# Kernel optimization log

Measured on AMD Instinct MI355X. Metric: run time of the kernel, lower is better.

Reference implementation:

```python
import jax, jax.numpy as jnp
import numpy as np

N_NODES = 100000


def _gcn_norm(edge_index, num_nodes):
    # PyG GCNConv default: add self-loops, symmetric normalization
    src, dst = edge_index[0], edge_index[1]
    loop = jnp.arange(num_nodes, dtype=src.dtype)
    src = jnp.concatenate([src, loop])
    dst = jnp.concatenate([dst, loop])
    deg = jax.ops.segment_sum(jnp.ones_like(dst, dtype=jnp.float32), dst,
                              num_segments=num_nodes)
    dinv = jnp.where(deg > 0, jax.lax.rsqrt(deg), 0.0)
    norm = dinv[src] * dinv[dst]  # [E + N]
    return src, dst, norm


def _gcn_conv(x, W, b, src, dst, norm, num_nodes):
    h = x @ W                                   # [N, out] linear first (PyG)
    msg = h[src] * norm[:, None]                # gather + scale  [E+N, out]
    out = jax.ops.segment_sum(msg, dst, num_segments=num_nodes)  # scatter-add
    return out + b


def setup_inputs() -> dict:
    key = jax.random.key(0)
    ks = jax.random.split(key, 5)
    x = jax.random.normal(ks[0], (N_NODES, 3), dtype=jnp.float32)
    edge_index = jax.random.randint(ks[1], (2, 1600000), 0, N_NODES, dtype=jnp.int64)
    # Glorot-ish weights, zero bias (PyG defaults)
    W1 = jax.random.normal(ks[2], (3, 64), dtype=jnp.float32) * (1.0 / np.sqrt(3))
    W2 = jax.random.normal(ks[3], (64, 64), dtype=jnp.float32) * (1.0 / np.sqrt(64))
    W3 = jax.random.normal(ks[4], (64, 3), dtype=jnp.float32) * (1.0 / np.sqrt(64))
    b1 = jnp.zeros((64,), jnp.float32)
    b2 = jnp.zeros((64,), jnp.float32)
    b3 = jnp.zeros((3,), jnp.float32)
    return {"x": x, "edge_index": edge_index, "W1": W1, "b1": b1,
            "W2": W2, "b2": b2, "W3": W3, "b3": b3}


def reference(x, edge_index, W1, b1, W2, b2, W3, b3):
    n = x.shape[0]
    src, dst, norm = _gcn_norm(edge_index, n)  # same graph for every layer
    h = jax.nn.relu(_gcn_conv(x, W1, b1, src, dst, norm, n))
    h = jax.nn.relu(_gcn_conv(h, W2, b2, src, dst, norm, n))
    return _gcn_conv(h, W3, b3, src, dst, norm, n)
```

## Files before the change

kernel.cpp:

```cpp
#include <hip/hip_runtime.h>

#define TPB 256
#define NB 391
#define CH 8192
#define BS 4736


__device__ __forceinline__ unsigned bpack(float a, float b) {
    unsigned ua = __float_as_uint(a), ub = __float_as_uint(b);
    ua = (ua + 0x7fffu + ((ua >> 16) & 1u)) >> 16;
    ub = (ub + 0x7fffu + ((ub >> 16) & 1u)) >> 16;
    return ua | (ub << 16);
}
__device__ __forceinline__ float blo(unsigned u) { return __uint_as_float(u << 16); }
__device__ __forceinline__ float bhi(unsigned u) { return __uint_as_float(u & 0xffff0000u); }


__global__ __launch_bounds__(512) void k_init(unsigned* __restrict__ gcur) {
    int t = threadIdx.x;
    if (t < NB) gcur[t] = (unsigned)(t * BS);
}


__global__ __launch_bounds__(TPB) void k_placeA(const int* __restrict__ src,
                                                const int* __restrict__ dst,
                                                unsigned* __restrict__ gcur,
                                                unsigned* __restrict__ bkt, int E) {
    __shared__ unsigned val[CH];
    __shared__ unsigned short bid[CH];
    __shared__ unsigned cnt[512], loff[512], lcur[512], basev[512];
    __shared__ unsigned tsum[TPB];
    int t = threadIdx.x;
    int c0 = blockIdx.x * CH;
    int n = E - c0; if (n > CH) n = CH;

    for (int b = t; b < 512; b += TPB) { cnt[b] = 0; lcur[b] = 0; }
    __syncthreads();
    for (int i = t; i < n; i += TPB)
        atomicAdd(&cnt[(unsigned)dst[c0 + i] >> 8], 1u);
    __syncthreads();
    for (int b = t; b < NB; b += TPB)
        basev[b] = cnt[b] ? atomicAdd(&gcur[b], cnt[b]) : 0u;
    unsigned a0 = cnt[2 * t], a1 = cnt[2 * t + 1];
    tsum[t] = a0 + a1;
    __syncthreads();
#pragma unroll
    for (int o = 1; o < TPB; o <<= 1) {
        unsigned v = (t >= o) ? tsum[t - o] : 0u;
        __syncthreads();
        tsum[t] += v;
        __syncthreads();
    }
    unsigned ex = tsum[t] - (a0 + a1);
    loff[2 * t] = ex; loff[2 * t + 1] = ex + a0;
    __syncthreads();
    for (int i = t; i < n; i += TPB) {
        unsigned s = (unsigned)src[c0 + i];
        unsigned d = (unsigned)dst[c0 + i];
        unsigned b = d >> 8;
        unsigned r = atomicAdd(&lcur[b], 1u);
        unsigned slot = loff[b] + r;
        val[slot] = s | ((d & 255u) << 20);
        bid[slot] = (unsigned short)b;
    }
    __syncthreads();
    for (int i = t; i < n; i += TPB) {
        unsigned b = bid[i];
        bkt[basev[b] + ((unsigned)i - loff[b])] = val[i];
    }
}


__global__ __launch_bounds__(TPB) void k_fineS(const unsigned* __restrict__ bkt,
                                               const unsigned* __restrict__ gcur,
                                               const float* __restrict__ x,
                                               int2* __restrict__ rp2,
                                               int* __restrict__ ssrc,
                                               float* __restrict__ dinv,
                                               float4* __restrict__ xs4, int N) {
    __shared__ unsigned cnt[256], sc[256], off[256];
    int t = threadIdx.x, b = blockIdx.x;
    cnt[t] = 0;
    __syncthreads();
    int p0 = b * BS, p1 = (int)gcur[b];
    for (int i = p0 + t; i < p1; i += TPB)
        atomicAdd(&cnt[bkt[i] >> 20], 1u);
    __syncthreads();
    unsigned c = cnt[t];
    sc[t] = c;
    __syncthreads();
#pragma unroll
    for (int o = 1; o < 256; o <<= 1) {
        unsigned v = (t >= o) ? sc[t - o] : 0u;
        __syncthreads();
        sc[t] += v;
        __syncthreads();
    }
    unsigned ex = sc[t] - c;
    off[t] = (unsigned)p0 + ex;
    int node = (b << 8) + t;
    if (node < N) {
        int beg = p0 + (int)ex;
        rp2[node] = make_int2(beg, beg + (int)c);
        float dv = rsqrtf((float)(c + 1u));
        dinv[node] = dv;
        float4 xv;
        xv.x = x[node * 3 + 0] * dv;
        xv.y = x[node * 3 + 1] * dv;
        xv.z = x[node * 3 + 2] * dv;
        xv.w = 0.f;
        xs4[node] = xv;
    }
    __syncthreads();
    for (int i = p0 + t; i < p1; i += TPB) {
        unsigned u = bkt[i];
        unsigned r = atomicAdd(&off[u >> 20], 1u);
        ssrc[r] = (int)(u & 0xFFFFFu);
    }
}


__global__ __launch_bounds__(TPB) void k_l1f2(const float4* __restrict__ xs4,
                                              const int2* __restrict__ rp2,
                                              const int* __restrict__ ssrc,
                                              const float* __restrict__ dinv,
                                              const float* __restrict__ W1,
                                              const float* __restrict__ b1,
                                              const float* __restrict__ W2,
                                              uint4* __restrict__ gb, int N) {
    int node = blockIdx.x * TPB + threadIdx.x;
    if (node >= N) return;
    int2 r = rp2[node];
    int beg = r.x, end = r.y;
    float4 q = xs4[node];
    int j = beg;
    for (; j + 3 < end; j += 4) {
        int s0 = ssrc[j], s1 = ssrc[j+1], s2 = ssrc[j+2], s3 = ssrc[j+3];
        float4 v0 = xs4[s0], v1 = xs4[s1], v2 = xs4[s2], v3 = xs4[s3];
        q.x += (v0.x + v1.x) + (v2.x + v3.x);
        q.y += (v0.y + v1.y) + (v2.y + v3.y);
        q.z += (v0.z + v1.z) + (v2.z + v3.z);
    }
    for (; j < end; ++j) {
        float4 v = xs4[ssrc[j]];
        q.x += v.x; q.y += v.y; q.z += v.z;
    }
    float dv = dinv[node];
    float q0 = q.x * dv, q1 = q.y * dv, q2 = q.z * dv;

    float acc[64];
#pragma unroll
    for (int f = 0; f < 64; ++f) acc[f] = 0.f;
    for (int kb = 0; kb < 16; ++kb) {
        int k0 = __builtin_amdgcn_readfirstlane(kb) << 2;
        const float* W1k = W1 + k0;
        const float* b1k = b1 + k0;
        float4 hv;
        hv.x = fmaxf(fmaf(q0, W1k[0], fmaf(q1, W1k[64], fmaf(q2, W1k[128], b1k[0]))), 0.f);
        hv.y = fmaxf(fmaf(q0, W1k[1], fmaf(q1, W1k[65], fmaf(q2, W1k[129], b1k[1]))), 0.f);
        hv.z = fmaxf(fmaf(q0, W1k[2], fmaf(q1, W1k[66], fmaf(q2, W1k[130], b1k[2]))), 0.f);
        hv.w = fmaxf(fmaf(q0, W1k[3], fmaf(q1, W1k[67], fmaf(q2, W1k[131], b1k[3]))), 0.f);
        const float* Wr = W2 + (k0 << 6);
#pragma unroll
        for (int f = 0; f < 64; ++f) {
            float a = acc[f];
            a = fmaf(hv.x, Wr[f],        a);
            a = fmaf(hv.y, Wr[64  + f],  a);
            a = fmaf(hv.z, Wr[128 + f],  a);
            a = fmaf(hv.w, Wr[192 + f],  a);
            acc[f] = a;
        }
    }
#pragma unroll
    for (int g8 = 0; g8 < 8; ++g8) {
        uint4 v;
        v.x = bpack(acc[8*g8+0] * dv, acc[8*g8+1] * dv);
        v.y = bpack(acc[8*g8+2] * dv, acc[8*g8+3] * dv);
        v.z = bpack(acc[8*g8+4] * dv, acc[8*g8+5] * dv);
        v.w = bpack(acc[8*g8+6] * dv, acc[8*g8+7] * dv);
        gb[((size_t)node << 3) + g8] = v;
    }
}


__global__ __launch_bounds__(TPB) void k_p2fb(const uint4* __restrict__ gb,
                                              const int2* __restrict__ rp2,
                                              const int* __restrict__ ssrc,
                                              const float* __restrict__ dinv,
                                              const float* __restrict__ b2,
                                              const float* __restrict__ W3,
                                              float* __restrict__ q4, int N) {
    int tid = blockIdx.x * TPB + threadIdx.x;
    int node = tid >> 3, q = tid & 7;
    if (node >= N) return;
    int2 r = rp2[node];
    int beg = r.x, end = r.y;
    float a[8];
    {
        uint4 u = gb[((size_t)node << 3) + q];
        a[0] = blo(u.x); a[1] = bhi(u.x);
        a[2] = blo(u.y); a[3] = bhi(u.y);
        a[4] = blo(u.z); a[5] = bhi(u.z);
        a[6] = blo(u.w); a[7] = bhi(u.w);
    }
    int j = beg;
    for (; j + 3 < end; j += 4) {
        int s0 = ssrc[j], s1 = ssrc[j+1], s2 = ssrc[j+2], s3 = ssrc[j+3];
        uint4 u0 = gb[((size_t)s0 << 3) + q];
        uint4 u1 = gb[((size_t)s1 << 3) + q];
        uint4 u2 = gb[((size_t)s2 << 3) + q];
        uint4 u3 = gb[((size_t)s3 << 3) + q];
        a[0] += (blo(u0.x) + blo(u1.x)) + (blo(u2.x) + blo(u3.x));
        a[1] += (bhi(u0.x) + bhi(u1.x)) + (bhi(u2.x) + bhi(u3.x));
        a[2] += (blo(u0.y) + blo(u1.y)) + (blo(u2.y) + blo(u3.y));
        a[3] += (bhi(u0.y) + bhi(u1.y)) + (bhi(u2.y) + bhi(u3.y));
        a[4] += (blo(u0.z) + blo(u1.z)) + (blo(u2.z) + blo(u3.z));
        a[5] += (bhi(u0.z) + bhi(u1.z)) + (bhi(u2.z) + bhi(u3.z));
        a[6] += (blo(u0.w) + blo(u1.w)) + (blo(u2.w) + blo(u3.w));
        a[7] += (bhi(u0.w) + bhi(u1.w)) + (bhi(u2.w) + bhi(u3.w));
    }
    for (; j < end; ++j) {
        uint4 u = gb[((size_t)ssrc[j] << 3) + q];
        a[0] += blo(u.x); a[1] += bhi(u.x);
        a[2] += blo(u.y); a[3] += bhi(u.y);
        a[4] += blo(u.z); a[5] += bhi(u.z);
        a[6] += blo(u.w); a[7] += bhi(u.w);
    }
    float dv = dinv[node];
    int f0 = q << 3;
    const float* bb = b2 + f0;
    const float* Wr = W3 + f0 * 3;
    float p0 = 0.f, p1 = 0.f, p2 = 0.f;
#pragma unroll
    for (int i = 0; i < 8; ++i) {
        float h = fmaxf(fmaf(a[i], dv, bb[i]), 0.f);
        p0 = fmaf(h, Wr[3*i+0], p0);
        p1 = fmaf(h, Wr[3*i+1], p1);
        p2 = fmaf(h, Wr[3*i+2], p2);
    }
#pragma unroll
    for (int off = 1; off < 8; off <<= 1) {
        p0 += __shfl_xor(p0, off, 64);
        p1 += __shfl_xor(p1, off, 64);
        p2 += __shfl_xor(p2, off, 64);
    }
    if (q < 4) {
        float v = (q == 0) ? p0 * dv : (q == 1) ? p1 * dv : (q == 2) ? p2 * dv : 0.f;
        q4[((size_t)node << 2) + q] = v;
    }
}


__global__ __launch_bounds__(TPB) void k_pull3o(const float* __restrict__ g34,
                                                const int2* __restrict__ rp2,
                                                const int* __restrict__ ssrc,
                                                const float* __restrict__ dinv,
                                                const float* __restrict__ b3,
                                                float* __restrict__ out, int N) {
    int tid = blockIdx.x * TPB + threadIdx.x;
    int node = tid >> 2, c = tid & 3;
    if (node >= N) return;
    int2 r = rp2[node];
    int beg = r.x, end = r.y;
    float acc = g34[tid];
    int j = beg;
    for (; j + 3 < end; j += 4) {
        int s0 = ssrc[j], s1 = ssrc[j+1], s2 = ssrc[j+2], s3 = ssrc[j+3];
        acc += (g34[(s0 << 2) + c] + g34[(s1 << 2) + c])
             + (g34[(s2 << 2) + c] + g34[(s3 << 2) + c]);
    }
    for (; j < end; ++j) acc += g34[(ssrc[j] << 2) + c];
    if (c < 3) out[(size_t)node * 3 + c] = dinv[node] * acc + b3[c];
}

extern "C" void kernel_launch(void* const* d_in, const int* in_sizes, int n_in,
                              void* d_out, int out_size, void* d_ws, size_t ws_size,
                              hipStream_t stream) {
    const float* x  = (const float*)d_in[0];
    const int*   ei = (const int*)  d_in[1];
    const float* W1 = (const float*)d_in[2];
    const float* b1 = (const float*)d_in[3];
    const float* W2 = (const float*)d_in[4];
    const float* b2 = (const float*)d_in[5];
    const float* W3 = (const float*)d_in[6];
    const float* b3 = (const float*)d_in[7];
    float* out = (float*)d_out;

    const int N = in_sizes[0] / 3;
    const int E = in_sizes[1] / 2;
    const int* srcI = ei;
    const int* dstI = ei + E;

    float*    ws   = (float*)d_ws;
    unsigned* gcur = (unsigned*)ws;
    int2*     rp2  = (int2*)    (ws + 512);
    float*    dinv = ws + 512 + 2 * (size_t)N;
    int*      ssrc = (int*)     (dinv + N);
    float*    xs4  = (float*)(ssrc + (size_t)NB * BS + 4);
    float*    q4   = xs4 + (size_t)N * 4;
    unsigned* gb   = (unsigned*)(q4 + (size_t)N * 4);
    unsigned* bkt  = gb + (size_t)N * 32;

    int gPlace = (E + CH - 1) / CH;
    int gS3    = (N * 4 + TPB - 1) / TPB;
    int gN     = (N + TPB - 1) / TPB;
    int gP2    = (int)(((size_t)N * 8 + TPB - 1) / TPB);

    k_init  <<<1,      512, 0, stream>>>(gcur);
    k_placeA<<<gPlace, TPB, 0, stream>>>(srcI, dstI, gcur, bkt, E);
    k_fineS <<<NB,     TPB, 0, stream>>>(bkt, gcur, x, rp2, ssrc, dinv,
                                         (float4*)xs4, N);

    k_l1f2<<<gN, TPB, 0, stream>>>((const float4*)xs4, rp2, ssrc, dinv,
                                   W1, b1, W2, (uint4*)gb, N);

    k_p2fb<<<gP2, TPB, 0, stream>>>((const uint4*)gb, rp2, ssrc, dinv,
                                    b2, W3, q4, N);

    k_pull3o<<<gS3, TPB, 0, stream>>>(q4, rp2, ssrc, dinv, b3, out, N);
}
```

Baseline: 226.7 us.

## Split layer-1 aggregate and W2 transform across four lanes per node

The fused layer-1 aggregation plus W2 matmul kernel now assigns four threads per node instead of one. Each lane gathers one channel of the neighbor features, the lanes exchange the aggregate via shuffles, and each lane computes 16 of the 64 outputs with W2 staged in shared memory. This cuts the per-thread register footprint from a 64-float accumulator and exposes four times more parallelism, which should improve occupancy. In exchange the neighbor gathers become scalar loads, the W1 transform is computed redundantly in all four lanes, and every block pays for a 16KB shared-memory load of W2.

```diff
diff --git a/kernel.cpp b/kernel.cpp
--- a/kernel.cpp
+++ b/kernel.cpp
@@ -120,66 +120,74 @@
 }
 
 
-__global__ __launch_bounds__(TPB) void k_l1f2(const float4* __restrict__ xs4,
-                                              const int2* __restrict__ rp2,
-                                              const int* __restrict__ ssrc,
-                                              const float* __restrict__ dinv,
-                                              const float* __restrict__ W1,
-                                              const float* __restrict__ b1,
-                                              const float* __restrict__ W2,
-                                              uint4* __restrict__ gb, int N) {
-    int node = blockIdx.x * TPB + threadIdx.x;
+__global__ __launch_bounds__(TPB) void k_l1q(const float* __restrict__ xs4,
+                                             const int2* __restrict__ rp2,
+                                             const int* __restrict__ ssrc,
+                                             const float* __restrict__ dinv,
+                                             const float* __restrict__ W1,
+                                             const float* __restrict__ b1,
+                                             const float* __restrict__ W2,
+                                             uint4* __restrict__ gb, int N) {
+    __shared__ float Ws[4096];
+    for (int i = threadIdx.x; i < 4096; i += TPB) Ws[i] = W2[i];
+    __syncthreads();
+    int tid = blockIdx.x * TPB + threadIdx.x;
+    int node = tid >> 2, c = tid & 3;
     if (node >= N) return;
     int2 r = rp2[node];
-    int beg = r.x, end = r.y;
-    float4 q = xs4[node];
-    int j = beg;
-    for (; j + 3 < end; j += 4) {
+    float acc = xs4[tid];
+    int j = r.x;
+    for (; j + 3 < r.y; j += 4) {
         int s0 = ssrc[j], s1 = ssrc[j+1], s2 = ssrc[j+2], s3 = ssrc[j+3];
-        float4 v0 = xs4[s0], v1 = xs4[s1], v2 = xs4[s2], v3 = xs4[s3];
-        q.x += (v0.x + v1.x) + (v2.x + v3.x);
-        q.y += (v0.y + v1.y) + (v2.y + v3.y);
-        q.z += (v0.z + v1.z) + (v2.z + v3.z);
-    }
-    for (; j < end; ++j) {
-        float4 v = xs4[ssrc[j]];
-        q.x += v.x; q.y += v.y; q.z += v.z;
-    }
+        acc += (xs4[(s0 << 2) + c] + xs4[(s1 << 2) + c])
+             + (xs4[(s2 << 2) + c] + xs4[(s3 << 2) + c]);
+    }
+    for (; j < r.y; ++j) acc += xs4[(ssrc[j] << 2) + c];
     float dv = dinv[node];
-    float q0 = q.x * dv, q1 = q.y * dv, q2 = q.z * dv;
-
-    float acc[64];
-#pragma unroll
-    for (int f = 0; f < 64; ++f) acc[f] = 0.f;
+    acc *= dv;
+    int base = (threadIdx.x & 63) & ~3;
+    float q0 = __shfl(acc, base + 0, 64);
+    float q1 = __shfl(acc, base + 1, 64);
+    float q2 = __shfl(acc, base + 2, 64);
+
+    float o[16];
+#pragma unroll
+    for (int i = 0; i < 16; ++i) o[i] = 0.f;
+    const int cofs = c << 4;
     for (int kb = 0; kb < 16; ++kb) {
         int k0 = __builtin_amdgcn_readfirstlane(kb) << 2;
         const float* W1k = W1 + k0;
         const float* b1k = b1 + k0;
-        float4 hv;
-        hv.x = fmaxf(fmaf(q0, W1k[0], fmaf(q1, W1k[64], fmaf(q2, W1k[128], b1k[0]))), 0.f);
-        hv.y = fmaxf(fmaf(q0, W1k[1], fmaf(q1, W1k[65], fmaf(q2, W1k[129], b1k[1]))), 0.f);
-        hv.z = fmaxf(fmaf(q0, W1k[2], fmaf(q1, W1k[66], fmaf(q2, W1k[130], b1k[2]))), 0.f);
-        hv.w = fmaxf(fmaf(q0, W1k[3], fmaf(q1, W1k[67], fmaf(q2, W1k[131], b1k[3]))), 0.f);
-        const float* Wr = W2 + (k0 << 6);
-#pragma unroll
-        for (int f = 0; f < 64; ++f) {
-            float a = acc[f];
-            a = fmaf(hv.x, Wr[f],        a);
-            a = fmaf(hv.y, Wr[64  + f],  a);
-            a = fmaf(hv.z, Wr[128 + f],  a);
-            a = fmaf(hv.w, Wr[192 + f],  a);
-            acc[f] = a;
+        float h[4];
+        h[0] = fmaxf(fmaf(q0, W1k[0], fmaf(q1, W1k[64], fmaf(q2, W1k[128], b1k[0]))), 0.f);
+        h[1] = fmaxf(fmaf(q0, W1k[1], fmaf(q1, W1k[65], fmaf(q2, W1k[129], b1k[1]))), 0.f);
+        h[2] = fmaxf(fmaf(q0, W1k[2], fmaf(q1, W1k[66], fmaf(q2, W1k[130], b1k[2]))), 0.f);
+        h[3] = fmaxf(fmaf(q0, W1k[3], fmaf(q1, W1k[67], fmaf(q2, W1k[131], b1k[3]))), 0.f);
+#pragma unroll
+        for (int kk = 0; kk < 4; ++kk) {
+            const float4* Wp = (const float4*)(Ws + ((k0 + kk) << 6) + cofs);
+#pragma unroll
+            for (int ii = 0; ii < 4; ++ii) {
+                float4 w = Wp[ii];
+                o[4*ii+0] = fmaf(h[kk], w.x, o[4*ii+0]);
+                o[4*ii+1] = fmaf(h[kk], w.y, o[4*ii+1]);
+                o[4*ii+2] = fmaf(h[kk], w.z, o[4*ii+2]);
+                o[4*ii+3] = fmaf(h[kk], w.w, o[4*ii+3]);
+            }
         }
     }
-#pragma unroll
-    for (int g8 = 0; g8 < 8; ++g8) {
-        uint4 v;
-        v.x = bpack(acc[8*g8+0] * dv, acc[8*g8+1] * dv);
-        v.y = bpack(acc[8*g8+2] * dv, acc[8*g8+3] * dv);
-        v.z = bpack(acc[8*g8+4] * dv, acc[8*g8+5] * dv);
-        v.w = bpack(acc[8*g8+6] * dv, acc[8*g8+7] * dv);
-        gb[((size_t)node << 3) + g8] = v;
-    }
+    uint4 v0, v1;
+    v0.x = bpack(o[0] * dv,  o[1] * dv);
+    v0.y = bpack(o[2] * dv,  o[3] * dv);
+    v0.z = bpack(o[4] * dv,  o[5] * dv);
+    v0.w = bpack(o[6] * dv,  o[7] * dv);
+    v1.x = bpack(o[8] * dv,  o[9] * dv);
+    v1.y = bpack(o[10] * dv, o[11] * dv);
+    v1.z = bpack(o[12] * dv, o[13] * dv);
+    v1.w = bpack(o[14] * dv, o[15] * dv);
+    uint4* gp = gb + ((size_t)node << 3) + (c << 1);
+    gp[0] = v0;
+    gp[1] = v1;
 }
 
 
@@ -303,7 +311,6 @@
 
     int gPlace = (E + CH - 1) / CH;
     int gS3    = (N * 4 + TPB - 1) / TPB;
-    int gN     = (N + TPB - 1) / TPB;
     int gP2    = (int)(((size_t)N * 8 + TPB - 1) / TPB);
 
     k_init  <<<1,      512, 0, stream>>>(gcur);
@@ -311,7 +318,7 @@
     k_fineS <<<NB,     TPB, 0, stream>>>(bkt, gcur, x, rp2, ssrc, dinv,
                                          (float4*)xs4, N);
 
-    k_l1f2<<<gN, TPB, 0, stream>>>((const float4*)xs4, rp2, ssrc, dinv,
+    k_l1q<<<gS3, TPB, 0, stream>>>(xs4, rp2, ssrc, dinv,
                                    W1, b1, W2, (uint4*)gb, N);
 
     k_p2fb<<<gP2, TPB, 0, stream>>>((const uint4*)gb, rp2, ssrc, dinv,
```

Result: faster. 211.3 us (-6.8%).
